# Optimization experiments

Measured on AMD Instinct MI355X. Metric: run time of the kernel, lower is better.

The kernel has to match this reference:

```python
import math
import jax, jax.numpy as jnp
import numpy as np

NUM_HEADS = 16
LN_EPS = 1e-5


def setup_inputs() -> dict:
    key = jax.random.key(0)
    ks = jax.random.split(key, 8)
    B, S, D = 2, 1024, 1024
    L, H = 4, NUM_HEADS
    hd = D // H
    return {
        "x": jax.random.normal(ks[0], (B, S, D), jnp.float32),
        "past_k": jax.random.normal(ks[1], (L, B, H, S, hd), jnp.float32),
        "past_v": jax.random.normal(ks[2], (L, B, H, S, hd), jnp.float32),
        "past_q": jax.random.normal(ks[3], (L, B, H, S, hd), jnp.float32),
        "Wqkv": jax.random.normal(ks[4], (3 * D, D), jnp.float32) * 0.02,
        "bqkv": jnp.zeros((3 * D,), jnp.float32),
        "Wout": jax.random.normal(ks[5], (D, D), jnp.float32) * 0.02,
        "bout": jnp.zeros((D,), jnp.float32),
    }


def reference(x, past_k, past_v, past_q, Wqkv, bqkv, Wout, bout):
    B, S, D = x.shape
    H = NUM_HEADS
    hd = D // H
    scale = 1.0 / math.sqrt(hd)

    # qkv projection + head split: [B,S,D] -> [B,H,S,hd] each
    qkv = x @ Wqkv.T + bqkv  # [B,S,3D]
    q, k, v = jnp.split(qkv, 3, axis=-1)
    split = lambda t: t.reshape(B, S, H, hd).transpose(0, 2, 1, 3)
    q, k, v = split(q), split(k), split(v)

    # causal token attention scores [B,H,S,S]
    token_scores = jnp.einsum("bhqd,bhkd->bhqk", q, k) * scale
    causal = jnp.triu(jnp.ones((S, S), bool), k=1)
    token_scores = jnp.where(causal, -jnp.inf, token_scores)

    # stack past layers: [L,B,H,S,hd] -> [B,S,L,D]
    def to_full(t):
        L = t.shape[0]
        return t.transpose(1, 3, 0, 2, 4).reshape(B, S, L, D)

    mem = jnp.concatenate([to_full(past_q), to_full(past_k), to_full(past_v)], axis=2)  # [B,S,M,D], M=3L
    M = mem.shape[2]

    # layer norm (no affine) over feature dim
    mu = mem.mean(-1, keepdims=True)
    var = mem.var(-1, keepdims=True)
    mem = (mem - mu) / jnp.sqrt(var + LN_EPS)

    # reproject through K/V slices of qkv weight
    Wk, bk = Wqkv[D:2 * D], bqkv[D:2 * D]
    Wv, bv = Wqkv[2 * D:], bqkv[2 * D:]
    rk = (mem @ Wk.T + bk).reshape(B, S, M, H, hd).transpose(0, 3, 1, 2, 4)  # [B,H,S,M,hd]
    rv = (mem @ Wv.T + bv).reshape(B, S, M, H, hd).transpose(0, 3, 1, 2, 4)

    # memory scores via per-position elementwise reduce [B,H,S,M]
    mem_scores = jnp.einsum("bhsd,bhsmd->bhsm", q, rk) * scale

    scores = jnp.concatenate([token_scores, mem_scores], axis=-1)  # [B,H,S,S+M]
    weights = jax.nn.softmax(scores, axis=-1)
    token_w, mem_w = weights[..., :S], weights[..., S:]

    token_ctx = jnp.einsum("bhqk,bhkd->bhqd", token_w, v)
    mem_ctx = jnp.einsum("bhsm,bhsmd->bhsd", mem_w, rv)
    attn = token_ctx + mem_ctx  # [B,H,S,hd]

    merged = attn.transpose(0, 2, 1, 3).reshape(B, S, D)
    out = merged @ Wout.T + bout
    return out, (k, v, q)
```

## Files before the change

kernel.cpp:

```cpp
#include <hip/hip_runtime.h>

#define BATCH 2
#define SEQ   1024
#define DIM   1024
#define NH    16
#define HD    64
#define NM    12
#define NTOK  (BATCH*SEQ)
#define MEMROWS (BATCH*SEQ*NM)
#define OUTT  2097152
#define NEGBIG (-1.0e30f)

typedef __attribute__((ext_vector_type(8))) short short8;
typedef __attribute__((ext_vector_type(4))) float f32x4;

__device__ __forceinline__ float bf2f(ushort u) {
    union { unsigned int i; float f; } t; t.i = ((unsigned int)u) << 16; return t.f;
}
__device__ __forceinline__ ushort f2bf(float f) {
    union { float f; unsigned int i; } t; t.f = f;
    unsigned int i = t.i;
    unsigned int lsb = (i >> 16) & 1u;
    i += 0x7fffu + lsb;
    return (ushort)(i >> 16);
}

__global__ __launch_bounds__(256) void cvt3_kernel(
    const float* __restrict__ a, ushort* __restrict__ ab, int na4,
    const float* __restrict__ b, ushort* __restrict__ bb, int nb4,
    const float* __restrict__ c, ushort* __restrict__ cb, int nc4)
{
    int i = blockIdx.x * 256 + threadIdx.x;
    if (i >= na4 + nb4 + nc4) return;
    const float* src; ushort* dst; int j;
    if (i < na4)            { src = a; dst = ab; j = i; }
    else if (i < na4 + nb4) { src = b; dst = bb; j = i - na4; }
    else                    { src = c; dst = cb; j = i - na4 - nb4; }
    float4 v = ((const float4*)src)[j];
    ushort4 o; o.x = f2bf(v.x); o.y = f2bf(v.y); o.z = f2bf(v.z); o.w = f2bf(v.w);
    ((ushort4*)dst)[j] = o;
}


__global__ __launch_bounds__(256) void mfma_qkv_kernel(
    const ushort* __restrict__ xb, const ushort* __restrict__ Wb,
    const float* __restrict__ bias, float* __restrict__ out,
    ushort* __restrict__ qkvb)
{
    __shared__ ushort As[128][40];
    __shared__ ushort Bs[128][40];
    const int tid = threadIdx.x;
    const int w = tid >> 6, lane = tid & 63;
    const int n = lane & 15, qd = lane >> 4;
    const int wr = (w >> 1) * 64, wc = (w & 1) * 64;
    const int row0 = blockIdx.y * 128, col0 = blockIdx.x * 128;
    const int r1 = tid >> 2, o1 = (tid & 3) * 8;
    const int r2 = (tid + 256) >> 2, o2 = ((tid + 256) & 3) * 8;

    f32x4 acc[4][4];
#pragma unroll
    for (int mt = 0; mt < 4; mt++)
#pragma unroll
        for (int nt = 0; nt < 4; nt++) acc[mt][nt] = (f32x4){0.f, 0.f, 0.f, 0.f};

    for (int k0 = 0; k0 < 1024; k0 += 32) {
        *(short8*)&As[r1][o1] = *(const short8*)(xb + (size_t)(row0 + r1) * 1024 + k0 + o1);
        *(short8*)&As[r2][o2] = *(const short8*)(xb + (size_t)(row0 + r2) * 1024 + k0 + o2);
        *(short8*)&Bs[r1][o1] = *(const short8*)(Wb + (size_t)(col0 + r1) * 1024 + k0 + o1);
        *(short8*)&Bs[r2][o2] = *(const short8*)(Wb + (size_t)(col0 + r2) * 1024 + k0 + o2);
        __syncthreads();
        short8 af[4], bf[4];
#pragma unroll
        for (int mt = 0; mt < 4; mt++) af[mt] = *(const short8*)&As[wr + mt * 16 + n][qd * 8];
#pragma unroll
        for (int nt = 0; nt < 4; nt++) bf[nt] = *(const short8*)&Bs[wc + nt * 16 + n][qd * 8];
#pragma unroll
        for (int mt = 0; mt < 4; mt++)
#pragma unroll
            for (int nt = 0; nt < 4; nt++)
                acc[mt][nt] = __builtin_amdgcn_mfma_f32_16x16x32_bf16(af[mt], bf[nt], acc[mt][nt], 0, 0, 0);
        __syncthreads();
    }
#pragma unroll
    for (int mt = 0; mt < 4; mt++)
#pragma unroll
        for (int nt = 0; nt < 4; nt++)
#pragma unroll
            for (int r = 0; r < 4; r++) {
                int row = row0 + wr + mt * 16 + qd * 4 + r;
                int col = col0 + wc + nt * 16 + n;
                float val = acc[mt][nt][r] + bias[col];
                int t = col >> 10, h = (col >> 6) & 15, d = col & 63;
                int b = row >> 10, s = row & 1023;
                size_t idx = (((size_t)(b * NH + h) * SEQ + s) * HD) + d;
                size_t base = (t == 0) ? (size_t)3 * OUTT : (t == 1) ? (size_t)OUTT : (size_t)2 * OUTT;
                out[base + idx] = val;
                qkvb[(size_t)t * OUTT + idx] = f2bf(val);
            }
}

__global__ __launch_bounds__(256) void mfma_out_kernel(
    const ushort* __restrict__ Ab, const ushort* __restrict__ Wb,
    const float* __restrict__ bias, float* __restrict__ C)
{
    __shared__ ushort As[128][40];
    __shared__ ushort Bs[128][40];
    const int tid = threadIdx.x;
    const int w = tid >> 6, lane = tid & 63;
    const int n = lane & 15, qd = lane >> 4;
    const int wr = (w >> 1) * 64, wc = (w & 1) * 64;
    const int row0 = blockIdx.y * 128, col0 = blockIdx.x * 128;
    const int r1 = tid >> 2, o1 = (tid & 3) * 8;
    const int r2 = (tid + 256) >> 2, o2 = ((tid + 256) & 3) * 8;

    f32x4 acc[4][4];
#pragma unroll
    for (int mt = 0; mt < 4; mt++)
#pragma unroll
        for (int nt = 0; nt < 4; nt++) acc[mt][nt] = (f32x4){0.f, 0.f, 0.f, 0.f};

    for (int k0 = 0; k0 < 1024; k0 += 32) {
        *(short8*)&As[r1][o1] = *(const short8*)(Ab + (size_t)(row0 + r1) * 1024 + k0 + o1);
        *(short8*)&As[r2][o2] = *(const short8*)(Ab + (size_t)(row0 + r2) * 1024 + k0 + o2);
        *(short8*)&Bs[r1][o1] = *(const short8*)(Wb + (size_t)(col0 + r1) * 1024 + k0 + o1);
        *(short8*)&Bs[r2][o2] = *(const short8*)(Wb + (size_t)(col0 + r2) * 1024 + k0 + o2);
        __syncthreads();
        short8 af[4], bf[4];
#pragma unroll
        for (int mt = 0; mt < 4; mt++) af[mt] = *(const short8*)&As[wr + mt * 16 + n][qd * 8];
#pragma unroll
        for (int nt = 0; nt < 4; nt++) bf[nt] = *(const short8*)&Bs[wc + nt * 16 + n][qd * 8];
#pragma unroll
        for (int mt = 0; mt < 4; mt++)
#pragma unroll
            for (int nt = 0; nt < 4; nt++)
                acc[mt][nt] = __builtin_amdgcn_mfma_f32_16x16x32_bf16(af[mt], bf[nt], acc[mt][nt], 0, 0, 0);
        __syncthreads();
    }
#pragma unroll
    for (int mt = 0; mt < 4; mt++)
#pragma unroll
        for (int nt = 0; nt < 4; nt++)
#pragma unroll
            for (int r = 0; r < 4; r++) {
                int row = row0 + wr + mt * 16 + qd * 4 + r;
                int col = col0 + wc + nt * 16 + n;
                C[(size_t)row * 1024 + col] = acc[mt][nt][r] + bias[col];
            }
}

__global__ __launch_bounds__(256) void mfma_qproj_kernel(
    const ushort* __restrict__ qkvb, const ushort* __restrict__ Wkb,
    ushort* __restrict__ qproj)
{
    __shared__ ushort As[128][40];
    __shared__ ushort Bs[128][40];
    const int tid = threadIdx.x;
    const int w = tid >> 6, lane = tid & 63;
    const int n = lane & 15, qd = lane >> 4;
    const int wr = (w >> 1) * 64, wc = (w & 1) * 64;
    const int row0 = blockIdx.y * 128, col0 = blockIdx.x * 128;
    const int h = blockIdx.z;
    const int b = row0 >> 10, s0 = row0 & 1023;
    const ushort* Abase = qkvb + ((size_t)(b * NH + h) * SEQ + s0) * HD;
    const int r1 = tid >> 2, o1 = (tid & 3) * 8;
    const int r2 = (tid + 256) >> 2, o2 = ((tid + 256) & 3) * 8;
    const int bkk = tid >> 3, bc0 = (tid & 7) * 16;

    f32x4 acc[4][4];
#pragma unroll
    for (int mt = 0; mt < 4; mt++)
#pragma unroll
        for (int nt = 0; nt < 4; nt++) acc[mt][nt] = (f32x4){0.f, 0.f, 0.f, 0.f};

    for (int k0 = 0; k0 < 64; k0 += 32) {
        *(short8*)&As[r1][o1] = *(const short8*)(Abase + (size_t)r1 * HD + k0 + o1);
        *(short8*)&As[r2][o2] = *(const short8*)(Abase + (size_t)r2 * HD + k0 + o2);
        {
            const ushort* bsrc = Wkb + (size_t)(h * HD + k0 + bkk) * 1024 + col0 + bc0;
            ushort tmp[16];
            *(short8*)&tmp[0] = *(const short8*)bsrc;
            *(short8*)&tmp[8] = *(const short8*)(bsrc + 8);
#pragma unroll
            for (int i = 0; i < 16; i++) Bs[bc0 + i][bkk] = tmp[i];
        }
        __syncthreads();
        short8 af[4], bf[4];
#pragma unroll
        for (int mt = 0; mt < 4; mt++) af[mt] = *(const short8*)&As[wr + mt * 16 + n][qd * 8];
#pragma unroll
        for (int nt = 0; nt < 4; nt++) bf[nt] = *(const short8*)&Bs[wc + nt * 16 + n][qd * 8];
#pragma unroll
        for (int mt = 0; mt < 4; mt++)
#pragma unroll
            for (int nt = 0; nt < 4; nt++)
                acc[mt][nt] = __builtin_amdgcn_mfma_f32_16x16x32_bf16(af[mt], bf[nt], acc[mt][nt], 0, 0, 0);
        __syncthreads();
    }
#pragma unroll
    for (int mt = 0; mt < 4; mt++)
#pragma unroll
        for (int nt = 0; nt < 4; nt++)
#pragma unroll
            for (int r = 0; r < 4; r++) {
                int token = row0 + wr + mt * 16 + qd * 4 + r;
                int col = col0 + wc + nt * 16 + n;
                qproj[((size_t)token * NH + h) * 1024 + col] = f2bf(acc[mt][nt][r]);
            }
}

__global__ __launch_bounds__(256) void mfma_vproj_kernel(
    const ushort* __restrict__ wvecb, const ushort* __restrict__ Wvb,
    const float* __restrict__ bv, const float* __restrict__ wmem,
    ushort* __restrict__ mergedb)
{
    __shared__ ushort As[128][40];
    __shared__ ushort Bs[64][40];
    const int tid = threadIdx.x;
    const int w = tid >> 6, lane = tid & 63;
    const int n = lane & 15, qd = lane >> 4;
    const int wr = (w >> 1) * 64, wc = (w & 1) * 32;
    const int row0 = blockIdx.x * 128;
    const int h = blockIdx.y;
    const int r1 = tid >> 2, o1 = (tid & 3) * 8;
    const int r2 = (tid + 256) >> 2, o2 = ((tid + 256) & 3) * 8;

    f32x4 acc[4][2];
#pragma unroll
    for (int mt = 0; mt < 4; mt++)
#pragma unroll
        for (int nt = 0; nt < 2; nt++) acc[mt][nt] = (f32x4){0.f, 0.f, 0.f, 0.f};

    for (int k0 = 0; k0 < 1024; k0 += 32) {
        *(short8*)&As[r1][o1] = *(const short8*)(wvecb + ((size_t)(row0 + r1) * NH + h) * 1024 + k0 + o1);
        *(short8*)&As[r2][o2] = *(const short8*)(wvecb + ((size_t)(row0 + r2) * NH + h) * 1024 + k0 + o2);
        *(short8*)&Bs[r1 & 63][o1] = *(const short8*)(Wvb + (size_t)(h * HD + (r1 & 63)) * 1024 + k0 + o1);
        __syncthreads();
        short8 af[4], bf[2];
#pragma unroll
        for (int mt = 0; mt < 4; mt++) af[mt] = *(const short8*)&As[wr + mt * 16 + n][qd * 8];
#pragma unroll
        for (int nt = 0; nt < 2; nt++) bf[nt] = *(const short8*)&Bs[wc + nt * 16 + n][qd * 8];
#pragma unroll
        for (int mt = 0; mt < 4; mt++)
#pragma unroll
            for (int nt = 0; nt < 2; nt++)
                acc[mt][nt] = __builtin_amdgcn_mfma_f32_16x16x32_bf16(af[mt], bf[nt], acc[mt][nt], 0, 0, 0);
        __syncthreads();
    }
#pragma unroll
    for (int mt = 0; mt < 4; mt++)
#pragma unroll
        for (int nt = 0; nt < 2; nt++)
#pragma unroll
            for (int r = 0; r < 4; r++) {
                int token = row0 + wr + mt * 16 + qd * 4 + r;
                int d = wc + nt * 16 + n;
                float ws = wmem[((size_t)token * NH + h) * 16 + 12];
                size_t mi = (size_t)token * DIM + h * HD + d;
                float val = bf2f(mergedb[mi]) + acc[mt][nt][r] + ws * bv[h * HD + d];
                mergedb[mi] = f2bf(val);
            }
}

__global__ __launch_bounds__(256) void msc_fused_kernel(
    const ushort* __restrict__ qproj, const ushort* __restrict__ mem_n,
    const ushort* __restrict__ qkvb, const float* __restrict__ bqkv,
    float* __restrict__ msc)
{
    const int tid = threadIdx.x;
    const int w = tid >> 6, lane = tid & 63;
    const int n = lane & 15, qd = lane >> 4;
    const int bs = blockIdx.x * 4 + w;

    float qbk = 0.f;
    if (lane < 16) {
        int b = bs >> 10, s = bs & 1023;
        const ushort* qrow = qkvb + ((size_t)(b * NH + lane) * SEQ + s) * HD;
        const float* bk = bqkv + DIM + lane * HD;
#pragma unroll
        for (int d = 0; d < HD; d++) qbk += bf2f(qrow[d]) * bk[d];
    }
    f32x4 acc = (f32x4){0.f, 0.f, 0.f, 0.f};
    const ushort* qpB = qproj + ((size_t)bs * NH + n) * 1024;
    const int mrow = (n < NM) ? n : 0;
    const ushort* mmB = mem_n + ((size_t)bs * NM + mrow) * 1024;
    for (int k0 = 0; k0 < 1024; k0 += 32) {
        short8 af = *(const short8*)(qpB + k0 + qd * 8);
        short8 bf = *(const short8*)(mmB + k0 + qd * 8);
        acc = __builtin_amdgcn_mfma_f32_16x16x32_bf16(af, bf, acc, 0, 0, 0);
    }
#pragma unroll
    for (int r = 0; r < 4; r++) {
        int h = qd * 4 + r;
        float qb = __shfl(qbk, h);
        if (n < NM)
            msc[((size_t)bs * NH + h) * NM + n] = 0.125f * (acc[r] + qb);
    }
}

__global__ __launch_bounds__(256) void ln_mem_kernel(
    const float* __restrict__ pq, const float* __restrict__ pk,
    const float* __restrict__ pv, ushort* __restrict__ mem_n)
{
    const int r = blockIdx.x;
    const int idx = r % NM;
    const int bs = r / NM;
    const int s = bs & (SEQ - 1);
    const int b = bs >> 10;
    const int c = idx >> 2;
    const int l = idx & 3;
    const float* src = (c == 0) ? pq : ((c == 1) ? pk : pv);
    const int tid = threadIdx.x;

    float vals[4];
    float sum = 0.f, sumsq = 0.f;
#pragma unroll
    for (int i = 0; i < 4; i++) {
        int dp = i * 256 + tid;
        int h = dp >> 6, d = dp & 63;
        float v = src[((((size_t)(l * BATCH + b) * NH + h) * SEQ + s) * HD) + d];
        vals[i] = v; sum += v; sumsq += v * v;
    }
    __shared__ float rs[256], rq[256];
    rs[tid] = sum; rq[tid] = sumsq;
    __syncthreads();
    for (int st = 128; st > 0; st >>= 1) {
        if (tid < st) { rs[tid] += rs[tid + st]; rq[tid] += rq[tid + st]; }
        __syncthreads();
    }
    float mu  = rs[0] * (1.f / 1024.f);
    float var = fmaxf(rq[0] * (1.f / 1024.f) - mu * mu, 0.f);
    float inv = rsqrtf(var + 1e-5f);
    ushort* dst = mem_n + (size_t)r * 1024;
#pragma unroll
    for (int i = 0; i < 4; i++) {
        int dp = i * 256 + tid;
        dst[dp] = f2bf((vals[i] - mu) * inv);
    }
}

#define TQ 64
#define TK 64
__global__ __launch_bounds__(256) void flash_attn_kernel(
    const ushort* __restrict__ qkvb, const float* __restrict__ msc,
    ushort* __restrict__ mergedb, float* __restrict__ wmem)
{
    __shared__ ushort Ks[TK][72];
    __shared__ ushort Vt[HD][72];
    __shared__ ushort Ps[4][16][72];

    const int bxr = blockIdx.x;
    const int qt = (bxr & 1) ? (bxr >> 1) : (15 - (bxr >> 1));
    const int bh = blockIdx.y;
    const int b = bh >> 4, h = bh & 15;
    const int tid = threadIdx.x;
    const int w = tid >> 6;
    const int lane = tid & 63;
    const int n = lane & 15;
    const int qd = lane >> 4;

    const ushort* qb = qkvb;
    const ushort* kb = qkvb + (size_t)OUTT;
    const ushort* vb = qkvb + (size_t)2 * OUTT;
    const size_t headoff = (size_t)bh * SEQ * HD;

    const int qrow0 = qt * TQ + w * 16;
    const ushort* qp = qb + headoff + (size_t)(qrow0 + n) * HD;
    short8 qf0 = *(const short8*)(qp + qd * 8);
    short8 qf1 = *(const short8*)(qp + 32 + qd * 8);

    float mrow[4], lrow[4];
    f32x4 Oacc[4];
#pragma unroll
    for (int r = 0; r < 4; r++) { mrow[r] = NEGBIG; lrow[r] = 0.f; }
#pragma unroll
    for (int nt = 0; nt < 4; nt++) Oacc[nt] = (f32x4){0.f, 0.f, 0.f, 0.f};

    for (int kt = 0; kt <= qt; kt++) {
        {
            int key = tid >> 2;
            int c0 = (tid & 3) * 16;
            const ushort* kg = kb + headoff + (size_t)(kt * TK + key) * HD + c0;
            *(short8*)&Ks[key][c0]     = *(const short8*)kg;
            *(short8*)&Ks[key][c0 + 8] = *(const short8*)(kg + 8);
            const ushort* vg = vb + headoff + (size_t)(kt * TK + key) * HD + c0;
            ushort vs[16];
            *(short8*)&vs[0] = *(const short8*)vg;
            *(short8*)&vs[8] = *(const short8*)(vg + 8);
#pragma unroll
            for (int i = 0; i < 16; i++) Vt[c0 + i][key] = vs[i];
        }
        __syncthreads();

        f32x4 sacc[4];
#pragma unroll
        for (int kc = 0; kc < 4; kc++) {
            short8 kf0 = *(const short8*)&Ks[kc * 16 + n][qd * 8];
            short8 kf1 = *(const short8*)&Ks[kc * 16 + n][32 + qd * 8];
            f32x4 z = (f32x4){0.f, 0.f, 0.f, 0.f};
            z = __builtin_amdgcn_mfma_f32_16x16x32_bf16(qf0, kf0, z, 0, 0, 0);
            z = __builtin_amdgcn_mfma_f32_16x16x32_bf16(qf1, kf1, z, 0, 0, 0);
            sacc[kc] = z;
        }
        const bool diag = (kt == qt);
#pragma unroll
        for (int kc = 0; kc < 4; kc++) {
#pragma unroll
            for (int r = 0; r < 4; r++) {
                float sv = sacc[kc][r] * 0.125f;
                if (diag) {
                    int qrow = qrow0 + qd * 4 + r;
                    int key = kt * TK + kc * 16 + n;
                    if (key > qrow) sv = NEGBIG;
                }
                sacc[kc][r] = sv;
            }
        }
        float alpha[4];
#pragma unroll
        for (int r = 0; r < 4; r++) {
            float mx = fmaxf(fmaxf(sacc[0][r], sacc[1][r]), fmaxf(sacc[2][r], sacc[3][r]));
            mx = fmaxf(mx, __shfl_xor(mx, 1));
            mx = fmaxf(mx, __shfl_xor(mx, 2));
            mx = fmaxf(mx, __shfl_xor(mx, 4));
            mx = fmaxf(mx, __shfl_xor(mx, 8));
            float mnew = fmaxf(mrow[r], mx);
            alpha[r] = __expf(mrow[r] - mnew);
            mrow[r] = mnew;
        }
        float psum[4] = {0.f, 0.f, 0.f, 0.f};
#pragma unroll
        for (int kc = 0; kc < 4; kc++) {
#pragma unroll
            for (int r = 0; r < 4; r++) {
                float p = __expf(sacc[kc][r] - mrow[r]);
                psum[r] += p;
                Ps[w][qd * 4 + r][kc * 16 + n] = f2bf(p);
            }
        }
#pragma unroll
        for (int r = 0; r < 4; r++) {
            float ps = psum[r];
            ps += __shfl_xor(ps, 1);
            ps += __shfl_xor(ps, 2);
            ps += __shfl_xor(ps, 4);
            ps += __shfl_xor(ps, 8);
            lrow[r] = alpha[r] * lrow[r] + ps;
        }
#pragma unroll
        for (int nt = 0; nt < 4; nt++)
#pragma unroll
            for (int r = 0; r < 4; r++)
                Oacc[nt][r] *= alpha[r];
        short8 pf0 = *(const short8*)&Ps[w][n][qd * 8];
        short8 pf1 = *(const short8*)&Ps[w][n][32 + qd * 8];
#pragma unroll
        for (int nt = 0; nt < 4; nt++) {
            short8 vf0 = *(const short8*)&Vt[nt * 16 + n][qd * 8];
            short8 vf1 = *(const short8*)&Vt[nt * 16 + n][32 + qd * 8];
            f32x4 z = Oacc[nt];
            z = __builtin_amdgcn_mfma_f32_16x16x32_bf16(pf0, vf0, z, 0, 0, 0);
            z = __builtin_amdgcn_mfma_f32_16x16x32_bf16(pf1, vf1, z, 0, 0, 0);
            Oacc[nt] = z;
        }
        __syncthreads();
    }

#pragma unroll
    for (int r = 0; r < 4; r++) {
        int srow = qrow0 + qd * 4 + r;
        const float* mp = msc + ((size_t)(b * SEQ + srow) * NH + h) * NM;
        float mm = NEGBIG;
#pragma unroll
        for (int j = 0; j < NM; j++) mm = fmaxf(mm, mp[j]);
        float mf = fmaxf(mrow[r], mm);
        float al = __expf(mrow[r] - mf);
        float msum = 0.f;
#pragma unroll
        for (int j = 0; j < NM; j++) msum += __expf(mp[j] - mf);
        float lf = al * lrow[r] + msum;
        float inv = 1.f / lf;
        float scale = al * inv;
        ushort* mrow_out = mergedb + (size_t)(b * SEQ + srow) * DIM + h * HD;
#pragma unroll
        for (int nt = 0; nt < 4; nt++)
            mrow_out[nt * 16 + n] = f2bf(Oacc[nt][r] * scale);
        size_t wb = ((size_t)(b * SEQ + srow) * NH + h) * 16;
        if (n < 12)       wmem[wb + n]  = __expf(mp[n] - mf) * inv;
        else if (n == 12) wmem[wb + 12] = msum * inv;
    }
}

__global__ __launch_bounds__(256) void wvec_kernel(
    const float* __restrict__ wmem, const ushort* __restrict__ mem_n,
    ushort* __restrict__ wvecb)
{
    __shared__ ushort memL[NM][1032];
    __shared__ float wL[NH][NM];
    const int bs = blockIdx.x;
    const int tid = threadIdx.x;

    for (int t = tid; t < NM * 256; t += 256) {
        int m = t >> 8, c4 = (t & 255) << 2;
        *(ushort4*)&memL[m][c4] = *(const ushort4*)(mem_n + ((size_t)bs * NM + m) * 1024 + c4);
    }
    if (tid < NH * NM) {
        int h = tid / NM, m = tid % NM;
        wL[h][m] = wmem[((size_t)bs * NH + h) * 16 + m];
    }
    __syncthreads();

    for (int h = 0; h < NH; h++) {
#pragma unroll
        for (int c0 = 0; c0 < 1024; c0 += 256) {
            int c = c0 + tid;
            float acc = 0.f;
#pragma unroll
            for (int m = 0; m < NM; m++)
                acc = fmaf(wL[h][m], bf2f(memL[m][c]), acc);
            wvecb[((size_t)bs * NH + h) * 1024 + c] = f2bf(acc);
        }
    }
}

extern "C" void kernel_launch(void* const* d_in, const int* in_sizes, int n_in,
                              void* d_out, int out_size, void* d_ws, size_t ws_size,
                              hipStream_t stream) {
    const float* x    = (const float*)d_in[0];
    const float* pk   = (const float*)d_in[1];
    const float* pv   = (const float*)d_in[2];
    const float* pq   = (const float*)d_in[3];
    const float* Wqkv = (const float*)d_in[4];
    const float* bqkv = (const float*)d_in[5];
    const float* Wout = (const float*)d_in[6];
    const float* bout = (const float*)d_in[7];
    float* out = (float*)d_out;

    ushort* mem_n  = (ushort*)d_ws;
    ushort* qproj  = mem_n + (size_t)MEMROWS * 1024;
    ushort* wvecb  = qproj;
    float*  msc    = (float*)(qproj + (size_t)NTOK * NH * 1024);
    float*  wmem   = msc + (size_t)NTOK * NH * NM;
    ushort* qkvb   = (ushort*)(wmem + (size_t)NTOK * NH * 16);
    ushort* Wqkvb  = qkvb + (size_t)3 * OUTT;
    ushort* Woutb  = Wqkvb + (size_t)3072 * 1024;
    ushort* xb     = Woutb + (size_t)1024 * 1024;
    ushort* mergedb = xb;

    const int na4 = NTOK * DIM / 4, nb4 = 3 * DIM * DIM / 4, nc4 = DIM * DIM / 4;

    cvt3_kernel<<<(na4 + nb4 + nc4 + 255) / 256, 256, 0, stream>>>(
        x, xb, na4, Wqkv, Wqkvb, nb4, Wout, Woutb, nc4);
    mfma_qkv_kernel<<<dim3(24, 16), 256, 0, stream>>>(xb, Wqkvb, bqkv, out, qkvb);
    ln_mem_kernel<<<MEMROWS, 256, 0, stream>>>(pq, pk, pv, mem_n);
    mfma_qproj_kernel<<<dim3(8, 16, NH), 256, 0, stream>>>(
        qkvb, Wqkvb + (size_t)DIM * DIM, qproj);
    msc_fused_kernel<<<NTOK / 4, 256, 0, stream>>>(qproj, mem_n, qkvb, bqkv, msc);
    flash_attn_kernel<<<dim3(16, 32), 256, 0, stream>>>(qkvb, msc, mergedb, wmem);
    wvec_kernel<<<NTOK, 256, 0, stream>>>(wmem, mem_n, wvecb);
    mfma_vproj_kernel<<<dim3(16, NH), 256, 0, stream>>>(
        wvecb, Wqkvb + (size_t)2 * DIM * DIM, bqkv + 2 * DIM, wmem, mergedb);
    mfma_out_kernel<<<dim3(8, 16), 256, 0, stream>>>(mergedb, Woutb, bout, out);
}
```

Baseline: 372.9 us.

## Split causal key tiles across two wave groups in flash attention

Flash attention blocks grow from 4 to 8 waves. Two groups of four waves process alternating key tiles, each with its own shared K/V buffers, and their running max/sum/accumulator states are combined through shared memory before the epilogue. This shortens the serial key loop per block, especially for the long diagonal query tiles, to improve latency and load balance. In exchange it costs more shared memory and registers per block, adds a merge step, and leaves the second group idle during the epilogue.

```diff
diff --git a/kernel.cpp b/kernel.cpp
--- a/kernel.cpp
+++ b/kernel.cpp
@@ -342,13 +342,15 @@
 
 #define TQ 64
 #define TK 64
-__global__ __launch_bounds__(256) void flash_attn_kernel(
+__global__ __launch_bounds__(512) void flash_attn_kernel(
     const ushort* __restrict__ qkvb, const float* __restrict__ msc,
     ushort* __restrict__ mergedb, float* __restrict__ wmem)
 {
-    __shared__ ushort Ks[TK][72];
-    __shared__ ushort Vt[HD][72];
-    __shared__ ushort Ps[4][16][72];
+    __shared__ __align__(16) char smem[55296];
+    ushort (*Ks)[TK][72]  = (ushort (*)[TK][72])smem;
+    ushort (*Vt)[HD][72]  = (ushort (*)[HD][72])(smem + 18432);
+    ushort (*Ps)[16][72]  = (ushort (*)[16][72])(smem + 36864);
+    float  (*cbuf)[64][25] = (float (*)[64][25])smem;
 
     const int bxr = blockIdx.x;
     const int qt = (bxr & 1) ? (bxr >> 1) : (15 - (bxr >> 1));
@@ -356,6 +358,8 @@
     const int b = bh >> 4, h = bh & 15;
     const int tid = threadIdx.x;
     const int w = tid >> 6;
+    const int g = w >> 2;
+    const int wq = w & 3;
     const int lane = tid & 63;
     const int n = lane & 15;
     const int qd = lane >> 4;
@@ -365,7 +369,7 @@
     const ushort* vb = qkvb + (size_t)2 * OUTT;
     const size_t headoff = (size_t)bh * SEQ * HD;
 
-    const int qrow0 = qt * TQ + w * 16;
+    const int qrow0 = qt * TQ + wq * 16;
     const ushort* qp = qb + headoff + (size_t)(qrow0 + n) * HD;
     short8 qf0 = *(const short8*)(qp + qd * 8);
     short8 qf1 = *(const short8*)(qp + 32 + qd * 8);
@@ -377,94 +381,128 @@
 #pragma unroll
     for (int nt = 0; nt < 4; nt++) Oacc[nt] = (f32x4){0.f, 0.f, 0.f, 0.f};
 
-    for (int kt = 0; kt <= qt; kt++) {
-        {
-            int key = tid >> 2;
-            int c0 = (tid & 3) * 16;
+    const int gtid = tid & 255;
+    const int key = gtid >> 2;
+    const int c0 = (gtid & 3) * 16;
+    const int nsteps = (qt + 2) >> 1;
+
+    for (int step = 0; step < nsteps; ++step) {
+        const int kt = 2 * step + g;
+        const bool act = (kt <= qt);
+        if (act) {
             const ushort* kg = kb + headoff + (size_t)(kt * TK + key) * HD + c0;
-            *(short8*)&Ks[key][c0]     = *(const short8*)kg;
-            *(short8*)&Ks[key][c0 + 8] = *(const short8*)(kg + 8);
+            *(short8*)&Ks[g][key][c0]     = *(const short8*)kg;
+            *(short8*)&Ks[g][key][c0 + 8] = *(const short8*)(kg + 8);
             const ushort* vg = vb + headoff + (size_t)(kt * TK + key) * HD + c0;
             ushort vs[16];
             *(short8*)&vs[0] = *(const short8*)vg;
             *(short8*)&vs[8] = *(const short8*)(vg + 8);
 #pragma unroll
-            for (int i = 0; i < 16; i++) Vt[c0 + i][key] = vs[i];
+            for (int i = 0; i < 16; i++) Vt[g][c0 + i][key] = vs[i];
         }
         __syncthreads();
-
-        f32x4 sacc[4];
-#pragma unroll
-        for (int kc = 0; kc < 4; kc++) {
-            short8 kf0 = *(const short8*)&Ks[kc * 16 + n][qd * 8];
-            short8 kf1 = *(const short8*)&Ks[kc * 16 + n][32 + qd * 8];
-            f32x4 z = (f32x4){0.f, 0.f, 0.f, 0.f};
-            z = __builtin_amdgcn_mfma_f32_16x16x32_bf16(qf0, kf0, z, 0, 0, 0);
-            z = __builtin_amdgcn_mfma_f32_16x16x32_bf16(qf1, kf1, z, 0, 0, 0);
-            sacc[kc] = z;
+        if (act) {
+            f32x4 sacc[4];
+#pragma unroll
+            for (int kc = 0; kc < 4; kc++) {
+                short8 kf0 = *(const short8*)&Ks[g][kc * 16 + n][qd * 8];
+                short8 kf1 = *(const short8*)&Ks[g][kc * 16 + n][32 + qd * 8];
+                f32x4 z = (f32x4){0.f, 0.f, 0.f, 0.f};
+                z = __builtin_amdgcn_mfma_f32_16x16x32_bf16(qf0, kf0, z, 0, 0, 0);
+                z = __builtin_amdgcn_mfma_f32_16x16x32_bf16(qf1, kf1, z, 0, 0, 0);
+                sacc[kc] = z;
+            }
+            const bool diag = (kt == qt);
+#pragma unroll
+            for (int kc = 0; kc < 4; kc++) {
+#pragma unroll
+                for (int r = 0; r < 4; r++) {
+                    float sv = sacc[kc][r] * 0.125f;
+                    if (diag) {
+                        int qrow = qrow0 + qd * 4 + r;
+                        int kk = kt * TK + kc * 16 + n;
+                        if (kk > qrow) sv = NEGBIG;
+                    }
+                    sacc[kc][r] = sv;
+                }
+            }
+            float alpha[4];
+#pragma unroll
+            for (int r = 0; r < 4; r++) {
+                float mx = fmaxf(fmaxf(sacc[0][r], sacc[1][r]), fmaxf(sacc[2][r], sacc[3][r]));
+                mx = fmaxf(mx, __shfl_xor(mx, 1));
+                mx = fmaxf(mx, __shfl_xor(mx, 2));
+                mx = fmaxf(mx, __shfl_xor(mx, 4));
+                mx = fmaxf(mx, __shfl_xor(mx, 8));
+                float mnew = fmaxf(mrow[r], mx);
+                alpha[r] = __expf(mrow[r] - mnew);
+                mrow[r] = mnew;
+            }
+            float psum[4] = {0.f, 0.f, 0.f, 0.f};
+#pragma unroll
+            for (int kc = 0; kc < 4; kc++) {
+#pragma unroll
+                for (int r = 0; r < 4; r++) {
+                    float p = __expf(sacc[kc][r] - mrow[r]);
+                    psum[r] += p;
+                    Ps[w][qd * 4 + r][kc * 16 + n] = f2bf(p);
+                }
+            }
+#pragma unroll
+            for (int r = 0; r < 4; r++) {
+                float ps = psum[r];
+                ps += __shfl_xor(ps, 1);
+                ps += __shfl_xor(ps, 2);
+                ps += __shfl_xor(ps, 4);
+                ps += __shfl_xor(ps, 8);
+                lrow[r] = alpha[r] * lrow[r] + ps;
+            }
+#pragma unroll
+            for (int nt = 0; nt < 4; nt++)
+#pragma unroll
+                for (int r = 0; r < 4; r++)
+                    Oacc[nt][r] *= alpha[r];
+            short8 pf0 = *(const short8*)&Ps[w][n][qd * 8];
+            short8 pf1 = *(const short8*)&Ps[w][n][32 + qd * 8];
+#pragma unroll
+            for (int nt = 0; nt < 4; nt++) {
+                short8 vf0 = *(const short8*)&Vt[g][nt * 16 + n][qd * 8];
+                short8 vf1 = *(const short8*)&Vt[g][nt * 16 + n][32 + qd * 8];
+                f32x4 z = Oacc[nt];
+                z = __builtin_amdgcn_mfma_f32_16x16x32_bf16(pf0, vf0, z, 0, 0, 0);
+                z = __builtin_amdgcn_mfma_f32_16x16x32_bf16(pf1, vf1, z, 0, 0, 0);
+                Oacc[nt] = z;
+            }
         }
-        const bool diag = (kt == qt);
-#pragma unroll
-        for (int kc = 0; kc < 4; kc++) {
-#pragma unroll
-            for (int r = 0; r < 4; r++) {
-                float sv = sacc[kc][r] * 0.125f;
-                if (diag) {
-                    int qrow = qrow0 + qd * 4 + r;
-                    int key = kt * TK + kc * 16 + n;
-                    if (key > qrow) sv = NEGBIG;
-                }
-                sacc[kc][r] = sv;
-            }
-        }
-        float alpha[4];
+        __syncthreads();
+    }
+
+    if (g == 1) {
+        float* cb = cbuf[wq][lane];
+#pragma unroll
+        for (int nt = 0; nt < 4; nt++)
+#pragma unroll
+            for (int r = 0; r < 4; r++) cb[nt * 4 + r] = Oacc[nt][r];
+#pragma unroll
+        for (int r = 0; r < 4; r++) { cb[16 + r] = mrow[r]; cb[20 + r] = lrow[r]; }
+    }
+    __syncthreads();
+    if (g == 1) return;
+
+    {
+        const float* cb = cbuf[wq][lane];
 #pragma unroll
         for (int r = 0; r < 4; r++) {
-            float mx = fmaxf(fmaxf(sacc[0][r], sacc[1][r]), fmaxf(sacc[2][r], sacc[3][r]));
-            mx = fmaxf(mx, __shfl_xor(mx, 1));
-            mx = fmaxf(mx, __shfl_xor(mx, 2));
-            mx = fmaxf(mx, __shfl_xor(mx, 4));
-            mx = fmaxf(mx, __shfl_xor(mx, 8));
-            float mnew = fmaxf(mrow[r], mx);
-            alpha[r] = __expf(mrow[r] - mnew);
+            float m1 = cb[16 + r], l1 = cb[20 + r];
+            float mnew = fmaxf(mrow[r], m1);
+            float a0 = __expf(mrow[r] - mnew);
+            float a1 = __expf(m1 - mnew);
+            lrow[r] = a0 * lrow[r] + a1 * l1;
+#pragma unroll
+            for (int nt = 0; nt < 4; nt++)
+                Oacc[nt][r] = a0 * Oacc[nt][r] + a1 * cb[nt * 4 + r];
             mrow[r] = mnew;
         }
-        float psum[4] = {0.f, 0.f, 0.f, 0.f};
-#pragma unroll
-        for (int kc = 0; kc < 4; kc++) {
-#pragma unroll
-            for (int r = 0; r < 4; r++) {
-                float p = __expf(sacc[kc][r] - mrow[r]);
-                psum[r] += p;
-                Ps[w][qd * 4 + r][kc * 16 + n] = f2bf(p);
-            }
-        }
-#pragma unroll
-        for (int r = 0; r < 4; r++) {
-            float ps = psum[r];
-            ps += __shfl_xor(ps, 1);
-            ps += __shfl_xor(ps, 2);
-            ps += __shfl_xor(ps, 4);
-            ps += __shfl_xor(ps, 8);
-            lrow[r] = alpha[r] * lrow[r] + ps;
-        }
-#pragma unroll
-        for (int nt = 0; nt < 4; nt++)
-#pragma unroll
-            for (int r = 0; r < 4; r++)
-                Oacc[nt][r] *= alpha[r];
-        short8 pf0 = *(const short8*)&Ps[w][n][qd * 8];
-        short8 pf1 = *(const short8*)&Ps[w][n][32 + qd * 8];
-#pragma unroll
-        for (int nt = 0; nt < 4; nt++) {
-            short8 vf0 = *(const short8*)&Vt[nt * 16 + n][qd * 8];
-            short8 vf1 = *(const short8*)&Vt[nt * 16 + n][32 + qd * 8];
-            f32x4 z = Oacc[nt];
-            z = __builtin_amdgcn_mfma_f32_16x16x32_bf16(pf0, vf0, z, 0, 0, 0);
-            z = __builtin_amdgcn_mfma_f32_16x16x32_bf16(pf1, vf1, z, 0, 0, 0);
-            Oacc[nt] = z;
-        }
-        __syncthreads();
     }
 
 #pragma unroll
@@ -557,7 +595,7 @@
     mfma_qproj_kernel<<<dim3(8, 16, NH), 256, 0, stream>>>(
         qkvb, Wqkvb + (size_t)DIM * DIM, qproj);
     msc_fused_kernel<<<NTOK / 4, 256, 0, stream>>>(qproj, mem_n, qkvb, bqkv, msc);
-    flash_attn_kernel<<<dim3(16, 32), 256, 0, stream>>>(qkvb, msc, mergedb, wmem);
+    flash_attn_kernel<<<dim3(16, 32), 512, 0, stream>>>(qkvb, msc, mergedb, wmem);
     wvec_kernel<<<NTOK, 256, 0, stream>>>(wmem, mem_n, wvecb);
     mfma_vproj_kernel<<<dim3(16, NH), 256, 0, stream>>>(
         wvecb, Wqkvb + (size_t)2 * DIM * DIM, bqkv + 2 * DIM, wmem, mergedb);
```

New measurement: 368.0 us. No clear change (-1.3%).
